# Kernel tuning notes

Hardware: AMD Instinct MI355X
Metric: run time of the kernel (lower is better)

Reference implementation:

```python
import jax, jax.numpy as jnp
import numpy as np

B, H, W, C, FD, HID = 64, 128, 128, 10, 32, 64
OFFSETS = [(-1,-1),(-1,0),(-1,1),(0,-1),(0,1),(1,-1),(1,0),(1,1)]

def setup_inputs() -> dict:
    key = jax.random.key(0)
    ks = jax.random.split(key, 13)
    s = lambda n: 1.0 / np.sqrt(n)
    return {
        "beliefs": jax.random.normal(ks[0], (B, H, W, C), jnp.float32),
        "constraints": jax.random.uniform(ks[1], (B, H, W, 8, 3), jnp.float32),
        "filename_embed": jax.random.normal(ks[2], (B, FD), jnp.float32),
        # message_net: Linear(2C+3+FD -> HID), ReLU, Linear(HID -> C)
        "mw1": jax.random.uniform(ks[3], (2*C+3+FD, HID), jnp.float32, -s(2*C+3+FD), s(2*C+3+FD)),
        "mb1": jax.random.uniform(ks[4], (HID,), jnp.float32, -s(2*C+3+FD), s(2*C+3+FD)),
        "mw2": jax.random.uniform(ks[5], (HID, C), jnp.float32, -s(HID), s(HID)),
        "mb2": jax.random.uniform(ks[6], (C,), jnp.float32, -s(HID), s(HID)),
        # update_net: Linear(2C -> HID), ReLU, Linear(HID -> C)
        "uw1": jax.random.uniform(ks[7], (2*C, HID), jnp.float32, -s(2*C), s(2*C)),
        "ub1": jax.random.uniform(ks[8], (HID,), jnp.float32, -s(2*C), s(2*C)),
        "uw2": jax.random.uniform(ks[9], (HID, C), jnp.float32, -s(HID), s(HID)),
        "ub2": jax.random.uniform(ks[10], (C,), jnp.float32, -s(HID), s(HID)),
        "gamma": jnp.ones((C,), jnp.float32),
        "beta": jnp.zeros((C,), jnp.float32),
    }

def reference(beliefs, constraints, filename_embed, mw1, mb1, mw2, mb2, uw1, ub1, uw2, ub2, gamma, beta):
    b, h, w, c = beliefs.shape
    # replicate-pad spatial dims (matches F.pad mode='replicate')
    bp = jnp.pad(beliefs, ((0,0),(1,1),(1,1),(0,0)), mode='edge')
    # gather 8 neighbors -> [B,H,W,8,C]
    neigh = jnp.stack([bp[:, 1+dy:1+dy+h, 1+dx:1+dx+w, :] for dy, dx in OFFSETS], axis=3)
    self_b = jnp.broadcast_to(beliefs[:, :, :, None, :], (b, h, w, 8, c))
    fn = jnp.broadcast_to(filename_embed[:, None, None, None, :], (b, h, w, 8, filename_embed.shape[-1]))
    msg_in = jnp.concatenate([self_b, neigh, constraints, fn], axis=-1)  # [B,H,W,8,2C+3+FD]
    msgs = jax.nn.relu(msg_in @ mw1 + mb1) @ mw2 + mb2                   # [B,H,W,8,C]
    agg = msgs.mean(axis=3)                                              # [B,H,W,C]
    upd_in = jnp.concatenate([beliefs, agg], axis=-1)
    upd = jax.nn.relu(upd_in @ uw1 + ub1) @ uw2 + ub2
    x = beliefs + 0.5 * upd
    mu = x.mean(-1, keepdims=True)
    var = ((x - mu) ** 2).mean(-1, keepdims=True)
    return (x - mu) * jax.lax.rsqrt(var + 1e-5) * gamma + beta
```

## Files before the change

### kernel.cpp

```cpp
#include <hip/hip_runtime.h>
#include <hip/hip_bf16.h>

typedef unsigned int u32;
typedef _Float16 h2 __attribute__((ext_vector_type(2)));

#define TILE 16
#define HALO 18
#define NPIX (HALO*HALO)

#define W_SELF   0
#define W_NBW    320
#define W_WC     640
#define W_MW2    736
#define W_UB1    1056
#define W_UW1    1088
#define W_UW2    1728
#define WS_W     2048
#define WS_SCAL  4096
#define WS_DWORDS 4136

__device__ __forceinline__ h2 pkrtz(float a, float b) {
    return __builtin_bit_cast(h2, __builtin_amdgcn_cvt_pkrtz(a, b));
}
#if __has_builtin(__builtin_elementwise_fma)
__device__ __forceinline__ h2 pkfma(h2 a, h2 b, h2 c) { return __builtin_elementwise_fma(a, b, c); }
#else
extern "C" __device__ h2 __ocml_fma_2f16(h2, h2, h2);
__device__ __forceinline__ h2 pkfma(h2 a, h2 b, h2 c) { return __ocml_fma_2f16(a, b, c); }
#endif
__device__ __forceinline__ float dot2f(h2 a, h2 b, float c) {
#if __has_builtin(__builtin_amdgcn_fdot2)
    return __builtin_amdgcn_fdot2(__builtin_bit_cast(__attribute__((ext_vector_type(2))) __fp16, a),
                                  __builtin_bit_cast(__attribute__((ext_vector_type(2))) __fp16, b),
                                  c, false);
#else
    return fmaf((float)a.x, (float)b.x, fmaf((float)a.y, (float)b.y, c));
#endif
}
__device__ __forceinline__ h2 relu2(h2 v) {
    h2 z = (h2)(_Float16)0;
#if __has_builtin(__builtin_elementwise_max)
    return __builtin_elementwise_max(v, z);
#else
    h2 r;
    r.x = v.x > (_Float16)0 ? v.x : (_Float16)0;
    r.y = v.y > (_Float16)0 ? v.y : (_Float16)0;
    return r;
#endif
}
__device__ __forceinline__ h2 h2cast(u32 v) { return __builtin_bit_cast(h2, v); }

__global__ __launch_bounds__(64) void prep_kernel(
    const float* __restrict__ fn,  const float* __restrict__ mw1, const float* __restrict__ mb1,
    const float* __restrict__ mw2, const float* __restrict__ mb2, const float* __restrict__ uw1,
    const float* __restrict__ ub1, const float* __restrict__ uw2, const float* __restrict__ ub2,
    const float* __restrict__ gam, const float* __restrict__ bet, u32* __restrict__ ws)
{
    const int b = blockIdx.x, t = threadIdx.x;
    h2* wh = (h2*)ws;
    if (t < 32) {
        float a0 = mb1[2*t], a1 = mb1[2*t+1];
        #pragma unroll 8
        for (int f = 0; f < 32; f++) {
            float fv = fn[b*32 + f];
            a0 += fv * mw1[(23+f)*64 + 2*t];
            a1 += fv * mw1[(23+f)*64 + 2*t+1];
        }
        wh[b*32 + t] = pkrtz(a0, a1);
    } else {
        const int i = b*32 + (t - 32);
        float a, c; int j;
        if      (i < 320)  { int cc = i>>5,  hp = i&31;  a = mw1[cc*64 + 2*hp];       c = mw1[cc*64 + 2*hp+1]; }
        else if (i < 640)  { j = i-320;  int q = j>>6, hh = j&63; a = mw1[(10+2*q)*64 + hh]; c = mw1[(11+2*q)*64 + hh]; }
        else if (i < 736)  { j = i-640;  int r = j>>5, hp = j&31; a = mw1[(20+r)*64 + 2*hp]; c = mw1[(20+r)*64 + 2*hp+1]; }
        else if (i < 1056) { j = i-736;  int cc = j>>5, hp = j&31; a = mw2[(2*hp)*10 + cc];  c = mw2[(2*hp+1)*10 + cc]; }
        else if (i < 1088) { j = i-1056; a = ub1[2*j]; c = ub1[2*j+1]; }
        else if (i < 1728) { j = i-1088; int cc = j>>5, hp = j&31; a = uw1[cc*64 + 2*hp];    c = uw1[cc*64 + 2*hp+1]; }
        else               { j = i-1728; int cc = j>>5, hp = j&31; a = uw2[(2*hp)*10 + cc];  c = uw2[(2*hp+1)*10 + cc]; }
        wh[WS_W + i] = pkrtz(a, c);
    }
    if (b == 0 && t < 40) {
        float v;
        if      (t < 10) v = mb2[t];
        else if (t < 20) v = ub2[t-10];
        else if (t < 30) v = gam[t-20];
        else             v = bet[t-30];
        ((float*)ws)[WS_SCAL + t] = v;
    }
}

__global__ __launch_bounds__(256, 6) void mp_kernel(
    const float* __restrict__ beliefs, const float* __restrict__ cons,
    const u32* __restrict__ ws, float* __restrict__ out)
{
    __shared__ __align__(16) u32 nbp_u[4*NPIX*4];

    const int tid = threadIdx.x;
    const int b = blockIdx.z, y0 = blockIdx.y*TILE, x0 = blockIdx.x*TILE;

    const h2* Wfnb = (const h2*)ws;
    const h2* W    = ((const h2*)ws) + WS_W;
    const float* SC = ((const float*)ws) + WS_SCAL;

    const int tx = tid & 15, ty = tid >> 4;
    const int pc = (ty+1)*HALO + (tx+1);
    const size_t gpix = (size_t)((b*128 + (y0+ty))*128 + (x0+tx));

    int pnb[8];
    {
        const int doff[8] = {-19,-18,-17,-1,1,17,18,19};
        #pragma unroll
        for (int k = 0; k < 8; k++) pnb[k] = pc + doff[k];
    }

    float bel[10]; h2 beld[10];
    {
        const float2* bp = (const float2*)(beliefs + gpix*10);
        #pragma unroll
        for (int q = 0; q < 5; q++) {
            float2 v = bp[q];
            bel[2*q] = v.x; bel[2*q+1] = v.y;
            beld[2*q]   = pkrtz(v.x, v.x);
            beld[2*q+1] = pkrtz(v.y, v.y);
        }
    }
    h2 cond[24];
    {
        const float4* cp = (const float4*)(cons + gpix*24);
        #pragma unroll
        for (int r = 0; r < 6; r++) {
            float4 v = cp[r];
            cond[4*r+0] = pkrtz(v.x, v.x);
            cond[4*r+1] = pkrtz(v.y, v.y);
            cond[4*r+2] = pkrtz(v.z, v.z);
            cond[4*r+3] = pkrtz(v.w, v.w);
        }
    }

    float acc2[10];
    #pragma unroll
    for (int c = 0; c < 10; c++) acc2[c] = 0.f;

    for (int half = 0; half < 2; half++) {
        if (half) __syncthreads();

        for (int p = tid; p < NPIX; p += 256) {
            int py = p/HALO, px = p - py*HALO;
            int gy = y0-1+py; gy = gy<0?0:(gy>127?127:gy);
            int gx = x0-1+px; gx = gx<0?0:(gx>127?127:gx);
            const float2* bp = (const float2*)(beliefs + (size_t)((b*128+gy)*128+gx)*10);
            h2 bc[5];
            #pragma unroll
            for (int q = 0; q < 5; q++) { float2 v = bp[q]; bc[q] = pkrtz(v.x, v.y); }
            #pragma unroll
            for (int cl = 0; cl < 4; cl++) {
                u32 ov[4];
                #pragma unroll
                for (int j = 0; j < 4; j++) {
                    const int hp = half*16 + cl*4 + j;
                    float a0 = 0.f, a1 = 0.f;
                    #pragma unroll
                    for (int q = 0; q < 5; q++) {
                        a0 = dot2f(bc[q], W[W_NBW + q*64 + 2*hp],     a0);
                        a1 = dot2f(bc[q], W[W_NBW + q*64 + 2*hp + 1], a1);
                    }
                    ov[j] = __builtin_bit_cast(u32, pkrtz(a0, a1));
                }
                *(uint4*)(nbp_u + ((cl*NPIX + p) << 2)) = make_uint4(ov[0], ov[1], ov[2], ov[3]);
            }
        }
        __syncthreads();

        #pragma unroll 2
        for (int cl = 0; cl < 4; cl++) {
            const int hb = half*16 + cl*4;
            h2 t01[4], s01[4];
            #pragma unroll
            for (int j = 0; j < 4; j++) { t01[j] = Wfnb[b*32 + hb + j]; s01[j] = (h2)(_Float16)0; }
            #pragma unroll
            for (int c = 0; c < 10; c++) {
                #pragma unroll
                for (int j = 0; j < 4; j++)
                    t01[j] = pkfma(beld[c], W[W_SELF + c*32 + hb + j], t01[j]);
            }
            h2 wc0[4], wc1[4], wc2[4];
            #pragma unroll
            for (int j = 0; j < 4; j++) {
                wc0[j] = W[W_WC      + hb + j];
                wc1[j] = W[W_WC + 32 + hb + j];
                wc2[j] = W[W_WC + 64 + hb + j];
            }
            #pragma unroll
            for (int k = 0; k < 8; k++) {
                const uint4 nv = *(const uint4*)(nbp_u + ((cl*NPIX + pnb[k]) << 2));
                const h2 nb[4] = { h2cast(nv.x), h2cast(nv.y), h2cast(nv.z), h2cast(nv.w) };
                const h2 c0 = cond[k*3+0], c1 = cond[k*3+1], c2 = cond[k*3+2];
                #pragma unroll
                for (int j = 0; j < 4; j++) {
                    h2 v = t01[j] + nb[j];
                    v = pkfma(c0, wc0[j], v);
                    v = pkfma(c1, wc1[j], v);
                    v = pkfma(c2, wc2[j], v);
                    s01[j] += relu2(v);
                }
            }
            #pragma unroll
            for (int c = 0; c < 10; c++) {
                #pragma unroll
                for (int j = 0; j < 4; j++)
                    acc2[c] = dot2f(s01[j], W[W_MW2 + c*32 + hb + j], acc2[c]);
            }
        }
    }

    h2 aggd[10];
    #pragma unroll
    for (int c = 0; c < 10; c++) {
        float a = acc2[c]*0.125f + SC[c];
        aggd[c] = pkrtz(a, a);
    }

    float od[10];
    #pragma unroll
    for (int c = 0; c < 10; c++) od[c] = 0.f;

    #pragma unroll 4
    for (int hp = 0; hp < 32; hp++) {
        h2 u01 = W[W_UB1 + hp];
        #pragma unroll
        for (int c = 0; c < 10; c++) u01 = pkfma(beld[c], W[W_UW1 + c*32 + hp], u01);
        #pragma unroll
        for (int c = 0; c < 10; c++) u01 = pkfma(aggd[c], W[W_UW1 + (10+c)*32 + hp], u01);
        u01 = relu2(u01);
        #pragma unroll
        for (int c = 0; c < 10; c++) od[c] = dot2f(u01, W[W_UW2 + c*32 + hp], od[c]);
    }

    float x[10], mu = 0.f;
    #pragma unroll
    for (int c = 0; c < 10; c++) { x[c] = bel[c] + 0.5f*(od[c] + SC[10+c]); mu += x[c]; }
    mu *= 0.1f;
    float var = 0.f;
    #pragma unroll
    for (int c = 0; c < 10; c++) { float d = x[c] - mu; var += d*d; }
    var *= 0.1f;
    const float rs = rsqrtf(var + 1e-5f);

    float2* op = (float2*)(out + gpix*10);
    #pragma unroll
    for (int q = 0; q < 5; q++) {
        float2 r;
        r.x = (x[2*q]   - mu)*rs*SC[20+2*q]   + SC[30+2*q];
        r.y = (x[2*q+1] - mu)*rs*SC[20+2*q+1] + SC[30+2*q+1];
        op[q] = r;
    }
}

__device__ __forceinline__ float bf_lo(u32 v) { return __uint_as_float(v << 16); }
__device__ __forceinline__ float bf_hi(u32 v) { return __uint_as_float(v & 0xffff0000u); }
__device__ __forceinline__ u32 f2bf(float f) {
    u32 u = __float_as_uint(f);
    return (u + 0x7fffu + ((u >> 16) & 1u)) >> 16;
}
__device__ __forceinline__ u32 pack2(float a, float b) { return f2bf(a) | (f2bf(b) << 16); }
__device__ __forceinline__ u32 fpair(const float* a, int pi) { return pack2(a[2*pi], a[2*pi+1]); }

#define FW_MW2 736
#define FW_MB2 1056
#define FW_UW1 1061
#define FW_UB1 1701
#define FW_UW2 1733
#define FW_UB2 2053
#define FW_GAM 2058
#define FW_BET 2063
#define FW_TOT 2068

__global__ __launch_bounds__(256) void fallback_kernel(
    const float* __restrict__ beliefs, const float* __restrict__ cons, const float* __restrict__ fn,
    const float* __restrict__ mw1, const float* __restrict__ mb1, const float* __restrict__ mw2,
    const float* __restrict__ mb2, const float* __restrict__ uw1, const float* __restrict__ ub1,
    const float* __restrict__ uw2, const float* __restrict__ ub2, const float* __restrict__ gam,
    const float* __restrict__ bet, float* __restrict__ out)
{
    __shared__ float bel_s[NPIX*10];
    __shared__ u32   nbp_s[32*NPIX];
    __shared__ u32   w_s[FW_TOT];
    __shared__ float fnb_s[64];

    const int tid = threadIdx.x;
    const int b  = blockIdx.z;
    const int y0 = blockIdx.y * TILE;
    const int x0 = blockIdx.x * TILE;

    for (int i = tid; i < FW_TOT; i += 256) {
        u32 v;
        if      (i < 736)  v = fpair(mw1, i);
        else if (i < 1056) v = fpair(mw2, i - 736);
        else if (i < 1061) v = fpair(mb2, i - 1056);
        else if (i < 1701) v = fpair(uw1, i - 1061);
        else if (i < 1733) v = fpair(ub1, i - 1701);
        else if (i < 2053) v = fpair(uw2, i - 1733);
        else if (i < 2058) v = fpair(ub2, i - 2053);
        else if (i < 2063) v = fpair(gam, i - 2058);
        else               v = fpair(bet, i - 2063);
        w_s[i] = v;
    }
    if (tid < 64) {
        float acc = mb1[tid];
        #pragma unroll 8
        for (int f = 0; f < 32; f++)
            acc += fn[b*32 + f] * mw1[(23 + f)*64 + tid];
        fnb_s[tid] = acc;
    }
    for (int idx = tid; idx < NPIX*10; idx += 256) {
        int p = idx/10, c = idx - p*10;
        int py = p/HALO, px = p - py*HALO;
        int gy = y0-1+py; gy = gy<0?0:(gy>127?127:gy);
        int gx = x0-1+px; gx = gx<0?0:(gx>127?127:gx);
        bel_s[idx] = beliefs[((size_t)(b*128+gy)*128+gx)*10 + c];
    }
    __syncthreads();

    for (int p = tid; p < NPIX; p += 256) {
        float bl[10];
        #pragma unroll
        for (int c = 0; c < 10; c++) bl[c] = bel_s[p*10 + c];
        #pragma unroll 4
        for (int hp = 0; hp < 32; hp++) {
            float t0 = 0.f, t1 = 0.f;
            #pragma unroll
            for (int c = 0; c < 10; c++) {
                u32 wv = w_s[(10 + c)*32 + hp];
                t0 += bl[c] * bf_lo(wv);
                t1 += bl[c] * bf_hi(wv);
            }
            nbp_s[hp*NPIX + p] = pack2(t0, t1);
        }
    }
    __syncthreads();

    const int tx = tid & 15, ty = tid >> 4;
    const int pc = (ty + 1)*HALO + (tx + 1);
    float bel[10];
    #pragma unroll
    for (int c = 0; c < 10; c++) bel[c] = bel_s[pc*10 + c];
    const size_t gpix = (size_t)(b*128 + (y0 + ty))*128 + (x0 + tx);
    float con[24];
    #pragma unroll
    for (int j = 0; j < 24; j++) con[j] = cons[gpix*24 + j];

    float acc2[10];
    #pragma unroll
    for (int c = 0; c < 10; c++) acc2[c] = 0.f;

    #pragma unroll 2
    for (int hp = 0; hp < 32; hp++) {
        const int h0 = 2*hp, h1 = h0 + 1;
        float t0 = fnb_s[h0], t1 = fnb_s[h1];
        #pragma unroll
        for (int c = 0; c < 10; c++) {
            u32 wv = w_s[c*32 + hp];
            t0 += bel[c] * bf_lo(wv);
            t1 += bel[c] * bf_hi(wv);
        }
        const u32 wc0 = w_s[20*32 + hp], wc1 = w_s[21*32 + hp], wc2 = w_s[22*32 + hp];
        const u32* nbb = nbp_s + hp*NPIX + pc - 19;
        float s0 = 0.f, s1 = 0.f;
        #pragma unroll
        for (int k = 0; k < 8; k++) {
            const int doff[8] = { 0, 1, 2, 18, 20, 36, 37, 38 };
            u32 nv = nbb[doff[k]];
            float c0 = con[k*3], c1 = con[k*3+1], c2 = con[k*3+2];
            float v0 = t0 + bf_lo(nv) + c0*bf_lo(wc0) + c1*bf_lo(wc1) + c2*bf_lo(wc2);
            float v1 = t1 + bf_hi(nv) + c0*bf_hi(wc0) + c1*bf_hi(wc1) + c2*bf_hi(wc2);
            s0 += fmaxf(v0, 0.f);
            s1 += fmaxf(v1, 0.f);
        }
        #pragma unroll
        for (int cq = 0; cq < 5; cq++) {
            u32 a0 = w_s[FW_MW2 + h0*5 + cq];
            u32 a1 = w_s[FW_MW2 + h1*5 + cq];
            acc2[2*cq]   += s0*bf_lo(a0) + s1*bf_lo(a1);
            acc2[2*cq+1] += s0*bf_hi(a0) + s1*bf_hi(a1);
        }
    }

    float agg[10];
    #pragma unroll
    for (int cq = 0; cq < 5; cq++) {
        u32 bp = w_s[FW_MB2 + cq];
        agg[2*cq]   = acc2[2*cq]  *0.125f + bf_lo(bp);
        agg[2*cq+1] = acc2[2*cq+1]*0.125f + bf_hi(bp);
    }

    float od[10];
    #pragma unroll
    for (int c = 0; c < 10; c++) od[c] = 0.f;
    #pragma unroll 2
    for (int hp = 0; hp < 32; hp++) {
        u32 ubp = w_s[FW_UB1 + hp];
        float u0 = bf_lo(ubp), u1 = bf_hi(ubp);
        #pragma unroll
        for (int c = 0; c < 10; c++) {
            u32 wv = w_s[FW_UW1 + c*32 + hp];
            u0 += bel[c] * bf_lo(wv);
            u1 += bel[c] * bf_hi(wv);
        }
        #pragma unroll
        for (int c = 0; c < 10; c++) {
            u32 wv = w_s[FW_UW1 + (10 + c)*32 + hp];
            u0 += agg[c] * bf_lo(wv);
            u1 += agg[c] * bf_hi(wv);
        }
        u0 = fmaxf(u0, 0.f); u1 = fmaxf(u1, 0.f);
        const int h0 = 2*hp, h1 = h0 + 1;
        #pragma unroll
        for (int cq = 0; cq < 5; cq++) {
            u32 a0 = w_s[FW_UW2 + h0*5 + cq];
            u32 a1 = w_s[FW_UW2 + h1*5 + cq];
            od[2*cq]   += u0*bf_lo(a0) + u1*bf_lo(a1);
            od[2*cq+1] += u0*bf_hi(a0) + u1*bf_hi(a1);
        }
    }

    float x[10], mu = 0.f;
    #pragma unroll
    for (int cq = 0; cq < 5; cq++) {
        u32 bp = w_s[FW_UB2 + cq];
        x[2*cq]   = bel[2*cq]   + 0.5f*(od[2*cq]   + bf_lo(bp));
        x[2*cq+1] = bel[2*cq+1] + 0.5f*(od[2*cq+1] + bf_hi(bp));
        mu += x[2*cq] + x[2*cq+1];
    }
    mu *= 0.1f;
    float var = 0.f;
    #pragma unroll
    for (int c = 0; c < 10; c++) { float d = x[c] - mu; var += d*d; }
    var *= 0.1f;
    const float rs = rsqrtf(var + 1e-5f);

    float2* op = reinterpret_cast<float2*>(out + gpix*10);
    #pragma unroll
    for (int q = 0; q < 5; q++) {
        u32 gp = w_s[FW_GAM + q], bq = w_s[FW_BET + q];
        float2 r;
        r.x = (x[2*q]   - mu)*rs*bf_lo(gp) + bf_lo(bq);
        r.y = (x[2*q+1] - mu)*rs*bf_hi(gp) + bf_hi(bq);
        op[q] = r;
    }
}

extern "C" void kernel_launch(void* const* d_in, const int* in_sizes, int n_in,
                              void* d_out, int out_size, void* d_ws, size_t ws_size,
                              hipStream_t stream) {
    (void)in_sizes; (void)n_in; (void)out_size;
    const float* beliefs = (const float*)d_in[0];
    const float* cons    = (const float*)d_in[1];
    const float* fn      = (const float*)d_in[2];
    const float* mw1     = (const float*)d_in[3];
    const float* mb1     = (const float*)d_in[4];
    const float* mw2     = (const float*)d_in[5];
    const float* mb2     = (const float*)d_in[6];
    const float* uw1     = (const float*)d_in[7];
    const float* ub1     = (const float*)d_in[8];
    const float* uw2     = (const float*)d_in[9];
    const float* ub2     = (const float*)d_in[10];
    const float* gam     = (const float*)d_in[11];
    const float* bet     = (const float*)d_in[12];
    float* outp = (float*)d_out;

    if (ws_size >= (size_t)WS_DWORDS*4) {
        prep_kernel<<<dim3(64), dim3(64), 0, stream>>>(
            fn, mw1, mb1, mw2, mb2, uw1, ub1, uw2, ub2, gam, bet, (u32*)d_ws);
        mp_kernel<<<dim3(8, 8, 64), dim3(256), 0, stream>>>(
            beliefs, cons, (const u32*)d_ws, outp);
    } else {
        fallback_kernel<<<dim3(8, 8, 64), dim3(256), 0, stream>>>(
            beliefs, cons, fn, mw1, mb1, mw2, mb2, uw1, ub1, uw2, ub2, gam, bet, outp);
    }
}
```

Baseline: 310.6 us.

## Split hidden units across two 256-thread groups with shared-memory reductions

Doubles the block to 512 threads. The two hidden-unit halves of the message MLP and the update MLP now run in parallel on separate thread groups instead of sequentially, and all neighbor projections are staged in shared memory in a single pass. Partial message accumulators and update outputs are combined through LDS with extra barriers, and only the first group writes output. This removes the per-thread serial half loop and one intermediate barrier, at the cost of doubling LDS use, adding reduction traffic, and possibly lowering occupancy under the 512x6 launch bounds.

```diff
diff --git a/kernel.cpp b/kernel.cpp
--- a/kernel.cpp
+++ b/kernel.cpp
@@ -89,11 +89,14 @@
     }
 }
 
-__global__ __launch_bounds__(256, 6) void mp_kernel(
+#define ACC_STRIDE 11
+#define OD_OFF (2*256*ACC_STRIDE)
+
+__global__ __launch_bounds__(512, 6) void mp_kernel(
     const float* __restrict__ beliefs, const float* __restrict__ cons,
     const u32* __restrict__ ws, float* __restrict__ out)
 {
-    __shared__ __align__(16) u32 nbp_u[4*NPIX*4];
+    __shared__ __align__(16) u32 nbp_u[8*NPIX*4];
 
     const int tid = threadIdx.x;
     const int b = blockIdx.z, y0 = blockIdx.y*TILE, x0 = blockIdx.x*TILE;
@@ -102,7 +105,36 @@
     const h2* W    = ((const h2*)ws) + WS_W;
     const float* SC = ((const float*)ws) + WS_SCAL;
 
-    const int tx = tid & 15, ty = tid >> 4;
+    for (int i = tid; i < 2*NPIX; i += 512) {
+        const int g2 = i & 1, p = i >> 1;
+        int py = p/HALO, px = p - py*HALO;
+        int gy = y0-1+py; gy = gy<0?0:(gy>127?127:gy);
+        int gx = x0-1+px; gx = gx<0?0:(gx>127?127:gx);
+        const float2* bp = (const float2*)(beliefs + (size_t)((b*128+gy)*128+gx)*10);
+        h2 bc[5];
+        #pragma unroll
+        for (int q = 0; q < 5; q++) { float2 v = bp[q]; bc[q] = pkrtz(v.x, v.y); }
+        #pragma unroll
+        for (int cl = 0; cl < 4; cl++) {
+            u32 ov[4];
+            #pragma unroll
+            for (int j = 0; j < 4; j++) {
+                const int hp = g2*16 + cl*4 + j;
+                float a0 = 0.f, a1 = 0.f;
+                #pragma unroll
+                for (int q = 0; q < 5; q++) {
+                    a0 = dot2f(bc[q], W[W_NBW + q*64 + 2*hp],     a0);
+                    a1 = dot2f(bc[q], W[W_NBW + q*64 + 2*hp + 1], a1);
+                }
+                ov[j] = __builtin_bit_cast(u32, pkrtz(a0, a1));
+            }
+            *(uint4*)(nbp_u + (((g2*4+cl)*NPIX + p) << 2)) = make_uint4(ov[0], ov[1], ov[2], ov[3]);
+        }
+    }
+    __syncthreads();
+
+    const int g = tid >> 8, lt = tid & 255;
+    const int tx = lt & 15, ty = lt >> 4;
     const int pc = (ty+1)*HALO + (tx+1);
     const size_t gpix = (size_t)((b*128 + (y0+ty))*128 + (x0+tx));
 
@@ -141,76 +173,57 @@
     #pragma unroll
     for (int c = 0; c < 10; c++) acc2[c] = 0.f;
 
-    for (int half = 0; half < 2; half++) {
-        if (half) __syncthreads();
-
-        for (int p = tid; p < NPIX; p += 256) {
-            int py = p/HALO, px = p - py*HALO;
-            int gy = y0-1+py; gy = gy<0?0:(gy>127?127:gy);
-            int gx = x0-1+px; gx = gx<0?0:(gx>127?127:gx);
-            const float2* bp = (const float2*)(beliefs + (size_t)((b*128+gy)*128+gx)*10);
-            h2 bc[5];
+    const int hbase = g*16;
+    #pragma unroll 2
+    for (int cl = 0; cl < 4; cl++) {
+        const int hb = hbase + cl*4;
+        h2 t01[4], s01[4];
+        #pragma unroll
+        for (int j = 0; j < 4; j++) { t01[j] = Wfnb[b*32 + hb + j]; s01[j] = (h2)(_Float16)0; }
+        #pragma unroll
+        for (int c = 0; c < 10; c++) {
             #pragma unroll
-            for (int q = 0; q < 5; q++) { float2 v = bp[q]; bc[q] = pkrtz(v.x, v.y); }
-            #pragma unroll
-            for (int cl = 0; cl < 4; cl++) {
-                u32 ov[4];
-                #pragma unroll
-                for (int j = 0; j < 4; j++) {
-                    const int hp = half*16 + cl*4 + j;
-                    float a0 = 0.f, a1 = 0.f;
-                    #pragma unroll
-                    for (int q = 0; q < 5; q++) {
-                        a0 = dot2f(bc[q], W[W_NBW + q*64 + 2*hp],     a0);
-                        a1 = dot2f(bc[q], W[W_NBW + q*64 + 2*hp + 1], a1);
-                    }
-                    ov[j] = __builtin_bit_cast(u32, pkrtz(a0, a1));
-                }
-                *(uint4*)(nbp_u + ((cl*NPIX + p) << 2)) = make_uint4(ov[0], ov[1], ov[2], ov[3]);
-            }
-        }
-        __syncthreads();
-
-        #pragma unroll 2
-        for (int cl = 0; cl < 4; cl++) {
-            const int hb = half*16 + cl*4;
-            h2 t01[4], s01[4];
-            #pragma unroll
-            for (int j = 0; j < 4; j++) { t01[j] = Wfnb[b*32 + hb + j]; s01[j] = (h2)(_Float16)0; }
-            #pragma unroll
-            for (int c = 0; c < 10; c++) {
-                #pragma unroll
-                for (int j = 0; j < 4; j++)
-                    t01[j] = pkfma(beld[c], W[W_SELF + c*32 + hb + j], t01[j]);
-            }
-            h2 wc0[4], wc1[4], wc2[4];
+            for (int j = 0; j < 4; j++)
+                t01[j] = pkfma(beld[c], W[W_SELF + c*32 + hb + j], t01[j]);
+        }
+        h2 wc0[4], wc1[4], wc2[4];
+        #pragma unroll
+        for (int j = 0; j < 4; j++) {
+            wc0[j] = W[W_WC      + hb + j];
+            wc1[j] = W[W_WC + 32 + hb + j];
+            wc2[j] = W[W_WC + 64 + hb + j];
+        }
+        #pragma unroll
+        for (int k = 0; k < 8; k++) {
+            const uint4 nv = *(const uint4*)(nbp_u + (((g*4+cl)*NPIX + pnb[k]) << 2));
+            const h2 nb[4] = { h2cast(nv.x), h2cast(nv.y), h2cast(nv.z), h2cast(nv.w) };
+            const h2 c0 = cond[k*3+0], c1 = cond[k*3+1], c2 = cond[k*3+2];
             #pragma unroll
             for (int j = 0; j < 4; j++) {
-                wc0[j] = W[W_WC      + hb + j];
-                wc1[j] = W[W_WC + 32 + hb + j];
-                wc2[j] = W[W_WC + 64 + hb + j];
+                h2 v = t01[j] + nb[j];
+                v = pkfma(c0, wc0[j], v);
+                v = pkfma(c1, wc1[j], v);
+                v = pkfma(c2, wc2[j], v);
+                s01[j] += relu2(v);
             }
+        }
+        #pragma unroll
+        for (int c = 0; c < 10; c++) {
             #pragma unroll
-            for (int k = 0; k < 8; k++) {
-                const uint4 nv = *(const uint4*)(nbp_u + ((cl*NPIX + pnb[k]) << 2));
-                const h2 nb[4] = { h2cast(nv.x), h2cast(nv.y), h2cast(nv.z), h2cast(nv.w) };
-                const h2 c0 = cond[k*3+0], c1 = cond[k*3+1], c2 = cond[k*3+2];
-                #pragma unroll
-                for (int j = 0; j < 4; j++) {
-                    h2 v = t01[j] + nb[j];
-                    v = pkfma(c0, wc0[j], v);
-                    v = pkfma(c1, wc1[j], v);
-                    v = pkfma(c2, wc2[j], v);
-                    s01[j] += relu2(v);
-                }
-            }
-            #pragma unroll
-            for (int c = 0; c < 10; c++) {
-                #pragma unroll
-                for (int j = 0; j < 4; j++)
-                    acc2[c] = dot2f(s01[j], W[W_MW2 + c*32 + hb + j], acc2[c]);
-            }
-        }
+            for (int j = 0; j < 4; j++)
+                acc2[c] = dot2f(s01[j], W[W_MW2 + c*32 + hb + j], acc2[c]);
+        }
+    }
+
+    __syncthreads();
+    float* xb = (float*)nbp_u;
+    #pragma unroll
+    for (int c = 0; c < 10; c++) xb[(g*256 + lt)*ACC_STRIDE + c] = acc2[c];
+    __syncthreads();
+    {
+        const float* ob = xb + ((1-g)*256 + lt)*ACC_STRIDE;
+        #pragma unroll
+        for (int c = 0; c < 10; c++) acc2[c] += ob[c];
     }
 
     h2 aggd[10];
@@ -225,7 +238,8 @@
     for (int c = 0; c < 10; c++) od[c] = 0.f;
 
     #pragma unroll 4
-    for (int hp = 0; hp < 32; hp++) {
+    for (int h = 0; h < 16; h++) {
+        const int hp = hbase + h;
         h2 u01 = W[W_UB1 + hp];
         #pragma unroll
         for (int c = 0; c < 10; c++) u01 = pkfma(beld[c], W[W_UW1 + c*32 + hp], u01);
@@ -236,23 +250,33 @@
         for (int c = 0; c < 10; c++) od[c] = dot2f(u01, W[W_UW2 + c*32 + hp], od[c]);
     }
 
-    float x[10], mu = 0.f;
-    #pragma unroll
-    for (int c = 0; c < 10; c++) { x[c] = bel[c] + 0.5f*(od[c] + SC[10+c]); mu += x[c]; }
-    mu *= 0.1f;
-    float var = 0.f;
-    #pragma unroll
-    for (int c = 0; c < 10; c++) { float d = x[c] - mu; var += d*d; }
-    var *= 0.1f;
-    const float rs = rsqrtf(var + 1e-5f);
-
-    float2* op = (float2*)(out + gpix*10);
-    #pragma unroll
-    for (int q = 0; q < 5; q++) {
-        float2 r;
-        r.x = (x[2*q]   - mu)*rs*SC[20+2*q]   + SC[30+2*q];
-        r.y = (x[2*q+1] - mu)*rs*SC[20+2*q+1] + SC[30+2*q+1];
-        op[q] = r;
+    if (g == 1) {
+        #pragma unroll
+        for (int c = 0; c < 10; c++) xb[OD_OFF + lt*ACC_STRIDE + c] = od[c];
+    }
+    __syncthreads();
+    if (g == 0) {
+        #pragma unroll
+        for (int c = 0; c < 10; c++) od[c] += xb[OD_OFF + lt*ACC_STRIDE + c];
+
+        float x[10], mu = 0.f;
+        #pragma unroll
+        for (int c = 0; c < 10; c++) { x[c] = bel[c] + 0.5f*(od[c] + SC[10+c]); mu += x[c]; }
+        mu *= 0.1f;
+        float var = 0.f;
+        #pragma unroll
+        for (int c = 0; c < 10; c++) { float d = x[c] - mu; var += d*d; }
+        var *= 0.1f;
+        const float rs = rsqrtf(var + 1e-5f);
+
+        float2* op = (float2*)(out + gpix*10);
+        #pragma unroll
+        for (int q = 0; q < 5; q++) {
+            float2 r;
+            r.x = (x[2*q]   - mu)*rs*SC[20+2*q]   + SC[30+2*q];
+            r.y = (x[2*q+1] - mu)*rs*SC[20+2*q+1] + SC[30+2*q+1];
+            op[q] = r;
+        }
     }
 }
 
@@ -471,7 +495,7 @@
     if (ws_size >= (size_t)WS_DWORDS*4) {
         prep_kernel<<<dim3(64), dim3(64), 0, stream>>>(
             fn, mw1, mb1, mw2, mb2, uw1, ub1, uw2, ub2, gam, bet, (u32*)d_ws);
-        mp_kernel<<<dim3(8, 8, 64), dim3(256), 0, stream>>>(
+        mp_kernel<<<dim3(8, 8, 64), dim3(512), 0, stream>>>(
             beliefs, cons, (const u32*)d_ws, outp);
     } else {
         fallback_kernel<<<dim3(8, 8, 64), dim3(256), 0, stream>>>(
```

Measured after the change: 798.0 us. 157% more time.
